# Optimization experiments

Measured on AMD Instinct MI355X. Metric: run time of the kernel, lower is better.

Reference implementation:

```python
import jax, jax.numpy as jnp
import numpy as np

IN_F, OUT_F, GROUP = 4096, 4096, 128
N_GROUPS = IN_F // GROUP  # 32


def setup_inputs() -> dict:
    key = jax.random.key(0)
    k1, k2, k3, k4, k5 = jax.random.split(key, 5)
    x = jax.random.normal(k1, (2, 1024, IN_F), dtype=jnp.float32)
    w_q = jax.random.randint(k2, (OUT_F, N_GROUPS, GROUP), -128, 128, dtype=jnp.int32)  # int8-range quantized weights
    s_w = jax.random.uniform(k3, (N_GROUPS, OUT_F), dtype=jnp.float32) * 0.01  # per-group, per-out-channel scales
    perm = jax.random.permutation(k4, IN_F).astype(jnp.int64)  # GPTQ activation-order permutation
    bias = jax.random.normal(k5, (OUT_F,), dtype=jnp.float32)
    return {"x": x, "w_q": w_q, "s_w": s_w, "perm": perm, "bias": bias}


def reference(x, w_q, s_w, perm, bias):
    prefix = x.shape[:-1]
    orig_dtype = x.dtype
    xf = x.reshape(-1, IN_F)          # (n, in)
    xf = xf[:, perm]                  # apply GPTQ permutation
    xf = xf.reshape(-1, N_GROUPS, GROUP).astype(jnp.float32)  # (n, g, k)
    wf = w_q.astype(jnp.float32)      # (o, g, k) dequant-to-fp32 weights (pre-scale)
    y_g = jnp.einsum('ngk,ogk->ngo', xf, wf)   # per-group partial products (n, g, o)
    y = jnp.sum(y_g * s_w[None, :, :], axis=1) # apply group scales, reduce groups -> (n, o)
    y = y + bias.astype(y.dtype)
    return y.reshape(*prefix, OUT_F).astype(orig_dtype)
```

## Files before the change

kernel.cpp:

```cpp
#include <hip/hip_runtime.h>
#include <hip/hip_bf16.h>
#include <stdint.h>

#define IN_F   4096
#define OUT_F  4096
#define M_ROWS 2048
#define NG     32
#define GRP    128

typedef int   v4i  __attribute__((ext_vector_type(4)));
typedef float f32x4 __attribute__((ext_vector_type(4)));

typedef const void __attribute__((address_space(1))) cv_g;
typedef void       __attribute__((address_space(3))) v_l;

__device__ __forceinline__ void async16(const void* g, void* l) {
  __builtin_amdgcn_global_load_lds((cv_g*)g, (v_l*)l, 16, 0, 0);
}

__device__ int g_perm_is64;

__global__ void decode_flag(const void* __restrict__ perm_raw) {
  if (threadIdx.x == 0 && blockIdx.x == 0) {
    const int* w = (const int*)perm_raw;
    int ok = 1;
    for (int j = 0; j < 32; ++j) {
      int lo = w[2 * j], hi = w[2 * j + 1];
      if (hi != 0 || lo < 0 || lo >= IN_F) { ok = 0; break; }
    }
    g_perm_is64 = ok;
  }
}

__global__ __launch_bounds__(256) void prep(const float* __restrict__ x,
                                            const int* __restrict__ w_q,
                                            const void* __restrict__ perm_raw,
                                            char* __restrict__ xq,
                                            char* __restrict__ w8,
                                            float* __restrict__ sxr) {
  __shared__ float sx[IN_F];
  __shared__ float red[4];
  __shared__ int sflag;
  const int b = blockIdx.x;
  const int t = threadIdx.x;

  if (b < M_ROWS) {
    const int m = b;
    const float* xr = x + (size_t)m * IN_F;
#pragma unroll
    for (int u = 0; u < 4; ++u) {
      int idx = (u * 256 + t) * 4;
      *(float4*)&sx[idx] = *(const float4*)&xr[idx];
    }
    if (t < 64) {
      const int* w = (const int*)perm_raw;
      int j = t & 31;
      int lo = w[2 * j], hi = w[2 * j + 1];
      int cond = (hi == 0 && lo >= 0 && lo < IN_F);
      unsigned long long bal = __ballot(cond);
      if (t == 0) sflag = (bal == ~0ull) ? 1 : 0;
    }
    __syncthreads();
    const int f = sflag;
    const long long* p64 = (const long long*)perm_raw;
    const int*       p32 = (const int*)perm_raw;
    const int jb = t * 16;
    float vals[16];
    float lmax = 0.f;
#pragma unroll
    for (int u = 0; u < 16; ++u) {
      int pj = f ? (int)p64[jb + u] : p32[jb + u];
      float v = sx[pj];
      vals[u] = v;
      lmax = fmaxf(lmax, fabsf(v));
    }
#pragma unroll
    for (int d = 1; d < 64; d <<= 1)
      lmax = fmaxf(lmax, __shfl_xor(lmax, d, 64));
    if ((t & 63) == 0) red[t >> 6] = lmax;
    __syncthreads();
    float rmax = fmaxf(fmaxf(red[0], red[1]), fmaxf(red[2], red[3]));
    float inv = (rmax > 0.f) ? 127.f / rmax : 0.f;
    if (t == 0) sxr[m] = rmax / 127.f;
    char q[16] __attribute__((aligned(16)));
#pragma unroll
    for (int u = 0; u < 16; ++u)
      q[u] = (char)__float2int_rn(vals[u] * inv);
    *(uint4*)(xq + (size_t)m * IN_F + jb) = *(const uint4*)q;
  } else {
    const int o  = b - M_ROWS;
    const int kb = t * 16;
    const int* wr = w_q + (size_t)o * IN_F + kb;
    int4 w0 = *(const int4*)(wr + 0);
    int4 w1 = *(const int4*)(wr + 4);
    int4 w2 = *(const int4*)(wr + 8);
    int4 w3 = *(const int4*)(wr + 12);
    char q[16] __attribute__((aligned(16)));
    q[0]=(char)w0.x; q[1]=(char)w0.y; q[2]=(char)w0.z; q[3]=(char)w0.w;
    q[4]=(char)w1.x; q[5]=(char)w1.y; q[6]=(char)w1.z; q[7]=(char)w1.w;
    q[8]=(char)w2.x; q[9]=(char)w2.y; q[10]=(char)w2.z; q[11]=(char)w2.w;
    q[12]=(char)w3.x; q[13]=(char)w3.y; q[14]=(char)w3.z; q[15]=(char)w3.w;
    *(uint4*)(w8 + (size_t)o * IN_F + kb) = *(const uint4*)q;
  }
}

__global__ __launch_bounds__(256, 2) void gemm_i8(
    const char* __restrict__ A,
    const char* __restrict__ B,
    const float* __restrict__ s_w,
    const float* __restrict__ sxr,
    const float* __restrict__ bias,
    float* __restrict__ C) {
  __shared__ char smem[2][32768];
  __shared__ unsigned short sws[NG * 128];

  const int tid  = threadIdx.x;
  const int wave = tid >> 6;
  const int lane = tid & 63;
  const int bm = blockIdx.y << 7;
  const int bn = blockIdx.x << 7;
  const int wm = (wave >> 1) << 6;
  const int wn = (wave & 1) << 6;
  const int lrow = lane & 15;
  const int quad = lane >> 4;

#pragma unroll
  for (int u = 0; u < 16; ++u) {
    int idx = u * 256 + tid;
    int g = idx >> 7, c = idx & 127;
    __hip_bfloat16 h = __float2bfloat16(s_w[(size_t)g * OUT_F + bn + c]);
    sws[idx] = *(unsigned short*)&h;
  }

  f32x4 accf[4][4] = {};

  const char* gp[8];
  int lofs[8];
#pragma unroll
  for (int h = 0; h < 8; ++h) {
    int c0 = (h * 4 + wave) * 64;
    int c  = c0 + lane;
    if (c < 1024) {
      int row = c >> 3;
      int kc  = (c & 7) ^ (row & 7);
      gp[h]   = A + (size_t)(bm + row) * IN_F + kc * 16;
      lofs[h] = c0 * 16;
    } else {
      int cb  = c - 1024;
      int row = cb >> 3;
      int kc  = (cb & 7) ^ (row & 7);
      gp[h]   = B + (size_t)(bn + row) * IN_F + kc * 16;
      lofs[h] = 16384 + (c0 - 1024) * 16;
    }
  }

  auto stage = [&](int p, int kn) {
#pragma unroll
    for (int h = 0; h < 8; ++h)
      async16(gp[h] + kn, &smem[p][lofs[h]]);
  };

  auto compute = [&](int p, int g) {
    const char* bufA = smem[p];
    const char* bufB = smem[p] + 16384;
    v4i acci[4][4] = {};
#pragma unroll
    for (int s = 0; s < 2; ++s) {
      v4i af[4], bf[4];
#pragma unroll
      for (int i = 0; i < 4; ++i) {
        int row = wm + i * 16 + lrow;
        af[i] = *(const v4i*)&bufA[row * 128 + (((s << 2) + quad) ^ (row & 7)) * 16];
      }
#pragma unroll
      for (int j = 0; j < 4; ++j) {
        int row = wn + j * 16 + lrow;
        bf[j] = *(const v4i*)&bufB[row * 128 + (((s << 2) + quad) ^ (row & 7)) * 16];
      }
#pragma unroll
      for (int i = 0; i < 4; ++i)
#pragma unroll
        for (int j = 0; j < 4; ++j)
          acci[i][j] = __builtin_amdgcn_mfma_i32_16x16x64_i8(af[i], bf[j], acci[i][j], 0, 0, 0);
    }
    float swv[4];
#pragma unroll
    for (int j = 0; j < 4; ++j) {
      unsigned int u = sws[g * 128 + wn + j * 16 + lrow];
      swv[j] = __uint_as_float(u << 16);
    }
#pragma unroll
    for (int i = 0; i < 4; ++i)
#pragma unroll
      for (int j = 0; j < 4; ++j)
#pragma unroll
        for (int r = 0; r < 4; ++r)
          accf[i][j][r] += swv[j] * (float)acci[i][j][r];
  };

  stage(0, 0);
  for (int k0 = 0; k0 < IN_F; k0 += 256) {
    __syncthreads();
    stage(1, k0 + 128);
    compute(0, k0 >> 7);
    __syncthreads();
    if (k0 + 256 < IN_F) stage(0, k0 + 256);
    compute(1, (k0 >> 7) + 1);
  }

#pragma unroll
  for (int i = 0; i < 4; ++i) {
    int r0 = bm + wm + i * 16 + quad * 4;
    float sxv[4];
#pragma unroll
    for (int r = 0; r < 4; ++r) sxv[r] = sxr[r0 + r];
#pragma unroll
    for (int j = 0; j < 4; ++j) {
      int col = bn + wn + j * 16 + lrow;
      float bv = bias[col];
#pragma unroll
      for (int r = 0; r < 4; ++r)
        C[(size_t)(r0 + r) * OUT_F + col] = sxv[r] * accf[i][j][r] + bv;
    }
  }
}

__global__ void naive_fallback(const float* __restrict__ x, const int* __restrict__ w_q,
                               const float* __restrict__ s_w, const void* __restrict__ perm_raw,
                               const float* __restrict__ bias, float* __restrict__ out) {
  int t = blockIdx.x * blockDim.x + threadIdx.x;
  int m = t >> 12;
  int o = t & 4095;
  const int f = g_perm_is64;
  const long long* p64 = (const long long*)perm_raw;
  const int*       p32 = (const int*)perm_raw;
  const float* xr = x + (size_t)m * IN_F;
  const int*   wr = w_q + (size_t)o * IN_F;
  float acc = 0.f;
  for (int g = 0; g < NG; ++g) {
    float part = 0.f;
    for (int k = 0; k < GRP; ++k) {
      int j = g * GRP + k;
      int pj = f ? (int)p64[j] : p32[j];
      part += xr[pj] * (float)wr[j];
    }
    acc += part * s_w[(size_t)g * OUT_F + o];
  }
  out[t] = acc + bias[o];
}

extern "C" void kernel_launch(void* const* d_in, const int* in_sizes, int n_in,
                              void* d_out, int out_size, void* d_ws, size_t ws_size,
                              hipStream_t stream) {
  const float* x    = (const float*)d_in[0];
  const int*   w_q  = (const int*)d_in[1];
  const float* s_w  = (const float*)d_in[2];
  const void*  perm = d_in[3];
  const float* bias = (const float*)d_in[4];
  float* out = (float*)d_out;

  const size_t xq_bytes = (size_t)M_ROWS * IN_F;
  const size_t w8_bytes = (size_t)OUT_F * IN_F;
  const size_t sx_bytes = (size_t)M_ROWS * sizeof(float);
  const size_t need = xq_bytes + w8_bytes + sx_bytes;

  if (ws_size < need) {
    decode_flag<<<1, 64, 0, stream>>>(perm);
    naive_fallback<<<(M_ROWS * OUT_F) / 256, 256, 0, stream>>>(x, w_q, s_w, perm, bias, out);
    return;
  }

  char*  xq  = (char*)d_ws;
  char*  w8  = (char*)d_ws + xq_bytes;
  float* sxr = (float*)((char*)d_ws + xq_bytes + w8_bytes);

  prep<<<M_ROWS + OUT_F, 256, 0, stream>>>(x, w_q, perm, xq, w8, sxr);

  dim3 grid(OUT_F / 128, M_ROWS / 128);
  gemm_i8<<<grid, 256, 0, stream>>>(xq, w8, s_w, sxr, bias, out);
}
```

Measured before the change: 193.0 us.

## Use 256x128 tiles with 512 threads and a triple-buffered async pipeline

```diff
diff --git a/kernel.cpp b/kernel.cpp
--- a/kernel.cpp
+++ b/kernel.cpp
@@ -7,6 +7,15 @@
 #define M_ROWS 2048
 #define NG     32
 #define GRP    128
+
+#define BM 256
+#define BN 128
+#define BK 128
+#define NTILES (IN_F / BK)
+#define ABYTES (BM * BK)
+#define BBYTES (BN * BK)
+#define BUFB   (ABYTES + BBYTES)
+#define ACHUNKS (ABYTES / 16)
 
 typedef int   v4i  __attribute__((ext_vector_type(4)));
 typedef float f32x4 __attribute__((ext_vector_type(4)));
@@ -104,20 +113,20 @@
   }
 }
 
-__global__ __launch_bounds__(256, 2) void gemm_i8(
+__global__ __launch_bounds__(512, 2) void gemm_i8(
     const char* __restrict__ A,
     const char* __restrict__ B,
     const float* __restrict__ s_w,
     const float* __restrict__ sxr,
     const float* __restrict__ bias,
     float* __restrict__ C) {
-  __shared__ char smem[2][32768];
-  __shared__ unsigned short sws[NG * 128];
+  __shared__ char smem[3][BUFB];
+  __shared__ unsigned short sws[NG * BN];
 
   const int tid  = threadIdx.x;
   const int wave = tid >> 6;
   const int lane = tid & 63;
-  const int bm = blockIdx.y << 7;
+  const int bm = blockIdx.y << 8;
   const int bn = blockIdx.x << 7;
   const int wm = (wave >> 1) << 6;
   const int wn = (wave & 1) << 6;
@@ -125,44 +134,51 @@
   const int quad = lane >> 4;
 
 #pragma unroll
-  for (int u = 0; u < 16; ++u) {
-    int idx = u * 256 + tid;
+  for (int u = 0; u < 8; ++u) {
+    int idx = u * 512 + tid;
     int g = idx >> 7, c = idx & 127;
     __hip_bfloat16 h = __float2bfloat16(s_w[(size_t)g * OUT_F + bn + c]);
     sws[idx] = *(unsigned short*)&h;
   }
 
-  f32x4 accf[4][4] = {};
-
-  const char* gp[8];
-  int lofs[8];
-#pragma unroll
-  for (int h = 0; h < 8; ++h) {
-    int c0 = (h * 4 + wave) * 64;
+  const char* gp[6];
+  int lofs[6];
+#pragma unroll
+  for (int h = 0; h < 6; ++h) {
+    int c0 = h * 512 + wave * 64;
     int c  = c0 + lane;
-    if (c < 1024) {
+    if (c0 < ACHUNKS) {
       int row = c >> 3;
       int kc  = (c & 7) ^ (row & 7);
       gp[h]   = A + (size_t)(bm + row) * IN_F + kc * 16;
       lofs[h] = c0 * 16;
     } else {
-      int cb  = c - 1024;
+      int cb  = c - ACHUNKS;
       int row = cb >> 3;
       int kc  = (cb & 7) ^ (row & 7);
       gp[h]   = B + (size_t)(bn + row) * IN_F + kc * 16;
-      lofs[h] = 16384 + (c0 - 1024) * 16;
-    }
-  }
-
-  auto stage = [&](int p, int kn) {
-#pragma unroll
-    for (int h = 0; h < 8; ++h)
-      async16(gp[h] + kn, &smem[p][lofs[h]]);
-  };
-
-  auto compute = [&](int p, int g) {
-    const char* bufA = smem[p];
-    const char* bufB = smem[p] + 16384;
+      lofs[h] = ABYTES + (c0 - ACHUNKS) * 16;
+    }
+  }
+
+  f32x4 accf[4][4] = {};
+
+#pragma unroll
+  for (int h = 0; h < 6; ++h) async16(gp[h], &smem[0][lofs[h]]);
+#pragma unroll
+  for (int h = 0; h < 6; ++h) async16(gp[h] + BK, &smem[1][lofs[h]]);
+  asm volatile("s_waitcnt vmcnt(6) lgkmcnt(0)" ::: "memory");
+  __builtin_amdgcn_s_barrier();
+  asm volatile("" ::: "memory");
+
+  int bufsel = 0;
+  for (int g = 0; g < NTILES; ++g) {
+    const char* bufA = smem[bufsel];
+    const char* bufB = bufA + ABYTES;
+    const int  stg   = (bufsel + 2 >= 3) ? bufsel - 1 : bufsel + 2;
+    const bool do_stage = (g + 2 < NTILES);
+    const int  kofs  = (g + 2) * BK;
+
     v4i acci[4][4] = {};
 #pragma unroll
     for (int s = 0; s < 2; ++s) {
@@ -170,23 +186,37 @@
 #pragma unroll
       for (int i = 0; i < 4; ++i) {
         int row = wm + i * 16 + lrow;
-        af[i] = *(const v4i*)&bufA[row * 128 + (((s << 2) + quad) ^ (row & 7)) * 16];
+        af[i] = *(const v4i*)&bufA[row * BK + ((((s << 2) + quad) ^ (row & 7)) << 4)];
       }
 #pragma unroll
       for (int j = 0; j < 4; ++j) {
         int row = wn + j * 16 + lrow;
-        bf[j] = *(const v4i*)&bufB[row * 128 + (((s << 2) + quad) ^ (row & 7)) * 16];
+        bf[j] = *(const v4i*)&bufB[row * BK + ((((s << 2) + quad) ^ (row & 7)) << 4)];
       }
+      if (do_stage) {
+#pragma unroll
+        for (int h = s * 3; h < s * 3 + 3; ++h)
+          async16(gp[h] + kofs, &smem[stg][lofs[h]]);
+      }
+      __builtin_amdgcn_s_barrier();
+      asm volatile("" ::: "memory");
+      __builtin_amdgcn_s_setprio(1);
 #pragma unroll
       for (int i = 0; i < 4; ++i)
 #pragma unroll
         for (int j = 0; j < 4; ++j)
           acci[i][j] = __builtin_amdgcn_mfma_i32_16x16x64_i8(af[i], bf[j], acci[i][j], 0, 0, 0);
-    }
+      __builtin_amdgcn_s_setprio(0);
+      if (s == 0) {
+        __builtin_amdgcn_s_barrier();
+        asm volatile("" ::: "memory");
+      }
+    }
+
     float swv[4];
 #pragma unroll
     for (int j = 0; j < 4; ++j) {
-      unsigned int u = sws[g * 128 + wn + j * 16 + lrow];
+      unsigned int u = sws[g * BN + wn + j * 16 + lrow];
       swv[j] = __uint_as_float(u << 16);
     }
 #pragma unroll
@@ -196,16 +226,14 @@
 #pragma unroll
         for (int r = 0; r < 4; ++r)
           accf[i][j][r] += swv[j] * (float)acci[i][j][r];
-  };
-
-  stage(0, 0);
-  for (int k0 = 0; k0 < IN_F; k0 += 256) {
-    __syncthreads();
-    stage(1, k0 + 128);
-    compute(0, k0 >> 7);
-    __syncthreads();
-    if (k0 + 256 < IN_F) stage(0, k0 + 256);
-    compute(1, (k0 >> 7) + 1);
+
+    if (g < NTILES - 1) {
+      if (g < NTILES - 2) asm volatile("s_waitcnt vmcnt(6)" ::: "memory");
+      else                asm volatile("s_waitcnt vmcnt(0)" ::: "memory");
+      __builtin_amdgcn_s_barrier();
+      asm volatile("" ::: "memory");
+    }
+    bufsel = (bufsel + 1 == 3) ? 0 : bufsel + 1;
   }
 
 #pragma unroll
@@ -276,6 +304,6 @@
 
   prep<<<M_ROWS + OUT_F, 256, 0, stream>>>(x, w_q, perm, xq, w8, sxr);
 
-  dim3 grid(OUT_F / 128, M_ROWS / 128);
-  gemm_i8<<<grid, 256, 0, stream>>>(xq, w8, s_w, sxr, bias, out);
-}
+  dim3 grid(OUT_F / BN, M_ROWS / BM);
+  gemm_i8<<<grid, 512, 0, stream>>>(xq, w8, s_w, sxr, bias, out);
+}
```

New measurement: 191.4 us. Within noise of the previous version (-0.8%).

## Restructure int8 GEMM main loop into a software-pipelined, single-barrier schedule

Applied to the files above, without the earlier changes.

```diff
diff --git a/kernel.cpp b/kernel.cpp
--- a/kernel.cpp
+++ b/kernel.cpp
@@ -111,8 +111,9 @@
     const float* __restrict__ sxr,
     const float* __restrict__ bias,
     float* __restrict__ C) {
-  __shared__ char smem[2][32768];
-  __shared__ unsigned short sws[NG * 128];
+  __shared__ __attribute__((aligned(16))) char lds[73728];
+  unsigned short* sws = (unsigned short*)lds;
+  const int BUF0 = 8192, BUF1 = 40960;
 
   const int tid  = threadIdx.x;
   const int wave = tid >> 6;
@@ -132,15 +133,13 @@
     sws[idx] = *(unsigned short*)&h;
   }
 
-  f32x4 accf[4][4] = {};
-
   const char* gp[8];
   int lofs[8];
 #pragma unroll
   for (int h = 0; h < 8; ++h) {
     int c0 = (h * 4 + wave) * 64;
     int c  = c0 + lane;
-    if (c < 1024) {
+    if (c0 < 1024) {
       int row = c >> 3;
       int kc  = (c & 7) ^ (row & 7);
       gp[h]   = A + (size_t)(bm + row) * IN_F + kc * 16;
@@ -154,35 +153,21 @@
     }
   }
 
-  auto stage = [&](int p, int kn) {
-#pragma unroll
-    for (int h = 0; h < 8; ++h)
-      async16(gp[h] + kn, &smem[p][lofs[h]]);
-  };
-
-  auto compute = [&](int p, int g) {
-    const char* bufA = smem[p];
-    const char* bufB = smem[p] + 16384;
-    v4i acci[4][4] = {};
-#pragma unroll
-    for (int s = 0; s < 2; ++s) {
-      v4i af[4], bf[4];
-#pragma unroll
-      for (int i = 0; i < 4; ++i) {
-        int row = wm + i * 16 + lrow;
-        af[i] = *(const v4i*)&bufA[row * 128 + (((s << 2) + quad) ^ (row & 7)) * 16];
-      }
-#pragma unroll
-      for (int j = 0; j < 4; ++j) {
-        int row = wn + j * 16 + lrow;
-        bf[j] = *(const v4i*)&bufB[row * 128 + (((s << 2) + quad) ^ (row & 7)) * 16];
-      }
-#pragma unroll
-      for (int i = 0; i < 4; ++i)
-#pragma unroll
-        for (int j = 0; j < 4; ++j)
-          acci[i][j] = __builtin_amdgcn_mfma_i32_16x16x64_i8(af[i], bf[j], acci[i][j], 0, 0, 0);
-    }
+  const int xlo = lrow & 7;
+  int aoff[2][4], boff[2][4];
+#pragma unroll
+  for (int s = 0; s < 2; ++s) {
+    int slot = (((s << 2) | quad) ^ xlo) << 4;
+#pragma unroll
+    for (int i = 0; i < 4; ++i) aoff[s][i] = (wm + i * 16 + lrow) * 128 + slot;
+#pragma unroll
+    for (int j = 0; j < 4; ++j) boff[s][j] = 16384 + (wn + j * 16 + lrow) * 128 + slot;
+  }
+
+  f32x4 accf[4][4] = {};
+  v4i   acci[4][4] = {};
+
+  auto rescale = [&](int g) {
     float swv[4];
 #pragma unroll
     for (int j = 0; j < 4; ++j) {
@@ -192,21 +177,58 @@
 #pragma unroll
     for (int i = 0; i < 4; ++i)
 #pragma unroll
-      for (int j = 0; j < 4; ++j)
+      for (int j = 0; j < 4; ++j) {
 #pragma unroll
         for (int r = 0; r < 4; ++r)
           accf[i][j][r] += swv[j] * (float)acci[i][j][r];
+        acci[i][j] = (v4i){0, 0, 0, 0};
+      }
   };
 
-  stage(0, 0);
-  for (int k0 = 0; k0 < IN_F; k0 += 256) {
-    __syncthreads();
-    stage(1, k0 + 128);
-    compute(0, k0 >> 7);
-    __syncthreads();
-    if (k0 + 256 < IN_F) stage(0, k0 + 256);
-    compute(1, (k0 >> 7) + 1);
-  }
+  auto tile = [&](int t, int pbase, int qbase, bool doPrev, bool doStage) {
+    v4i af0[4], bf0[4], af1[4], bf1[4];
+#pragma unroll
+    for (int i = 0; i < 4; ++i) af0[i] = *(const v4i*)&lds[pbase + aoff[0][i]];
+#pragma unroll
+    for (int j = 0; j < 4; ++j) bf0[j] = *(const v4i*)&lds[pbase + boff[0][j]];
+#pragma unroll
+    for (int i = 0; i < 4; ++i) af1[i] = *(const v4i*)&lds[pbase + aoff[1][i]];
+#pragma unroll
+    for (int j = 0; j < 4; ++j) bf1[j] = *(const v4i*)&lds[pbase + boff[1][j]];
+    if (doStage) {
+      const int kn = (t + 1) * GRP;
+#pragma unroll
+      for (int h = 0; h < 8; ++h) async16(gp[h] + kn, &lds[qbase + lofs[h]]);
+    }
+    if (doPrev) rescale(t - 1);
+    __builtin_amdgcn_s_setprio(1);
+#pragma unroll
+    for (int i = 0; i < 4; ++i)
+#pragma unroll
+      for (int j = 0; j < 4; ++j)
+        acci[i][j] = __builtin_amdgcn_mfma_i32_16x16x64_i8(af0[i], bf0[j], acci[i][j], 0, 0, 0);
+#pragma unroll
+    for (int i = 0; i < 4; ++i)
+#pragma unroll
+      for (int j = 0; j < 4; ++j)
+        acci[i][j] = __builtin_amdgcn_mfma_i32_16x16x64_i8(af1[i], bf1[j], acci[i][j], 0, 0, 0);
+    __builtin_amdgcn_s_setprio(0);
+    if (doStage) asm volatile("s_waitcnt vmcnt(0)" ::: "memory");
+    __builtin_amdgcn_s_barrier();
+    asm volatile("" ::: "memory");
+  };
+
+#pragma unroll
+  for (int h = 0; h < 8; ++h) async16(gp[h], &lds[BUF0 + lofs[h]]);
+  asm volatile("s_waitcnt vmcnt(0) lgkmcnt(0)" ::: "memory");
+  __builtin_amdgcn_s_barrier();
+  asm volatile("" ::: "memory");
+
+  for (int it = 0; it < 16; ++it) {
+    tile(2 * it,     BUF0, BUF1, it > 0, true);
+    tile(2 * it + 1, BUF1, BUF0, true,   it < 15);
+  }
+  rescale(NG - 1);
 
 #pragma unroll
   for (int i = 0; i < 4; ++i) {
```

New measurement: 212.5 us. 1.1x slower.

## Load B fragments directly to registers and software-pipeline the int8 GEMM main loop

Applied to the files above, without the earlier changes.

```diff
diff --git a/kernel.cpp b/kernel.cpp
--- a/kernel.cpp
+++ b/kernel.cpp
@@ -111,8 +111,9 @@
     const float* __restrict__ sxr,
     const float* __restrict__ bias,
     float* __restrict__ C) {
-  __shared__ char smem[2][32768];
-  __shared__ unsigned short sws[NG * 128];
+  __shared__ __attribute__((aligned(16))) char lds[40960];
+  unsigned short* sws = (unsigned short*)lds;
+  const int BUF0 = 8192, BUF1 = 24576;
 
   const int tid  = threadIdx.x;
   const int wave = tid >> 6;
@@ -132,57 +133,23 @@
     sws[idx] = *(unsigned short*)&h;
   }
 
-  f32x4 accf[4][4] = {};
-
-  const char* gp[8];
-  int lofs[8];
-#pragma unroll
-  for (int h = 0; h < 8; ++h) {
+  const char* gp[4];
+  int lofs[4];
+#pragma unroll
+  for (int h = 0; h < 4; ++h) {
     int c0 = (h * 4 + wave) * 64;
     int c  = c0 + lane;
-    if (c < 1024) {
-      int row = c >> 3;
-      int kc  = (c & 7) ^ (row & 7);
-      gp[h]   = A + (size_t)(bm + row) * IN_F + kc * 16;
-      lofs[h] = c0 * 16;
-    } else {
-      int cb  = c - 1024;
-      int row = cb >> 3;
-      int kc  = (cb & 7) ^ (row & 7);
-      gp[h]   = B + (size_t)(bn + row) * IN_F + kc * 16;
-      lofs[h] = 16384 + (c0 - 1024) * 16;
-    }
-  }
-
-  auto stage = [&](int p, int kn) {
-#pragma unroll
-    for (int h = 0; h < 8; ++h)
-      async16(gp[h] + kn, &smem[p][lofs[h]]);
-  };
-
-  auto compute = [&](int p, int g) {
-    const char* bufA = smem[p];
-    const char* bufB = smem[p] + 16384;
-    v4i acci[4][4] = {};
-#pragma unroll
-    for (int s = 0; s < 2; ++s) {
-      v4i af[4], bf[4];
-#pragma unroll
-      for (int i = 0; i < 4; ++i) {
-        int row = wm + i * 16 + lrow;
-        af[i] = *(const v4i*)&bufA[row * 128 + (((s << 2) + quad) ^ (row & 7)) * 16];
-      }
-#pragma unroll
-      for (int j = 0; j < 4; ++j) {
-        int row = wn + j * 16 + lrow;
-        bf[j] = *(const v4i*)&bufB[row * 128 + (((s << 2) + quad) ^ (row & 7)) * 16];
-      }
-#pragma unroll
-      for (int i = 0; i < 4; ++i)
-#pragma unroll
-        for (int j = 0; j < 4; ++j)
-          acci[i][j] = __builtin_amdgcn_mfma_i32_16x16x64_i8(af[i], bf[j], acci[i][j], 0, 0, 0);
-    }
+    int row = c >> 3;
+    int kc  = (c & 7) ^ (row & 7);
+    gp[h]   = A + (size_t)(bm + row) * IN_F + kc * 16;
+    lofs[h] = c0 * 16;
+  }
+
+  f32x4 accf[4][4] = {};
+  v4i   acci[4][4] = {};
+  v4i   bfX[2][4], bfY[2][4];
+
+  auto rescale = [&](int g) {
     float swv[4];
 #pragma unroll
     for (int j = 0; j < 4; ++j) {
@@ -192,21 +159,76 @@
 #pragma unroll
     for (int i = 0; i < 4; ++i)
 #pragma unroll
-      for (int j = 0; j < 4; ++j)
+      for (int j = 0; j < 4; ++j) {
 #pragma unroll
         for (int r = 0; r < 4; ++r)
           accf[i][j][r] += swv[j] * (float)acci[i][j][r];
+        acci[i][j] = (v4i){0, 0, 0, 0};
+      }
   };
 
-  stage(0, 0);
-  for (int k0 = 0; k0 < IN_F; k0 += 256) {
-    __syncthreads();
-    stage(1, k0 + 128);
-    compute(0, k0 >> 7);
-    __syncthreads();
-    if (k0 + 256 < IN_F) stage(0, k0 + 256);
-    compute(1, (k0 >> 7) + 1);
-  }
+  const char* Brow = B + (size_t)(bn + wn + lrow) * IN_F + (quad << 4);
+
+#define TILE(T, PB, QB, BC, BN_, DOPREV, DOSTAGE)                              \
+  {                                                                            \
+    if (DOSTAGE) {                                                             \
+      const int kn = (T + 1) * GRP;                                            \
+      _Pragma("unroll")                                                        \
+      for (int h = 0; h < 4; ++h) async16(gp[h] + kn, &lds[QB + lofs[h]]);     \
+      __builtin_amdgcn_sched_barrier(0);                                       \
+      _Pragma("unroll")                                                        \
+      for (int s = 0; s < 2; ++s)                                              \
+        _Pragma("unroll")                                                      \
+        for (int j = 0; j < 4; ++j)                                            \
+          BN_[s][j] = *(const v4i*)(Brow + (size_t)(j * 16) * IN_F +           \
+                                    (T + 1) * GRP + (s << 6));                 \
+      __builtin_amdgcn_sched_barrier(0);                                       \
+    }                                                                          \
+    if (DOPREV) rescale((T) - 1);                                              \
+    _Pragma("unroll")                                                          \
+    for (int s = 0; s < 2; ++s) {                                              \
+      v4i af[4];                                                               \
+      _Pragma("unroll")                                                        \
+      for (int i = 0; i < 4; ++i) {                                            \
+        int row = wm + i * 16 + lrow;                                          \
+        af[i] = *(const v4i*)&lds[PB + row * 128 +                             \
+                                  ((((s << 2) | quad) ^ (lrow & 7)) << 4)];    \
+      }                                                                        \
+      __builtin_amdgcn_s_setprio(1);                                           \
+      _Pragma("unroll")                                                        \
+      for (int i = 0; i < 4; ++i)                                              \
+        _Pragma("unroll")                                                      \
+        for (int j = 0; j < 4; ++j)                                            \
+          acci[i][j] = __builtin_amdgcn_mfma_i32_16x16x64_i8(                  \
+              af[i], BC[s][j], acci[i][j], 0, 0, 0);                           \
+      __builtin_amdgcn_s_setprio(0);                                           \
+    }                                                                          \
+    if (DOSTAGE) {                                                             \
+      asm volatile("s_waitcnt vmcnt(8)" ::: "memory");                         \
+      __builtin_amdgcn_s_barrier();                                            \
+      asm volatile("" ::: "memory");                                           \
+    }                                                                          \
+  }
+
+#pragma unroll
+  for (int h = 0; h < 4; ++h) async16(gp[h], &lds[BUF0 + lofs[h]]);
+  __builtin_amdgcn_sched_barrier(0);
+#pragma unroll
+  for (int s = 0; s < 2; ++s)
+#pragma unroll
+    for (int j = 0; j < 4; ++j)
+      bfX[s][j] = *(const v4i*)(Brow + (size_t)(j * 16) * IN_F + (s << 6));
+  __builtin_amdgcn_sched_barrier(0);
+  asm volatile("s_waitcnt vmcnt(8) lgkmcnt(0)" ::: "memory");
+  __builtin_amdgcn_s_barrier();
+  asm volatile("" ::: "memory");
+
+  for (int it = 0; it < 16; ++it) {
+    TILE(2 * it,     BUF0, BUF1, bfX, bfY, (it > 0), true);
+    TILE(2 * it + 1, BUF1, BUF0, bfY, bfX, true,     (it < 15));
+  }
+  rescale(NG - 1);
+#undef TILE
 
 #pragma unroll
   for (int i = 0; i < 4; ++i) {
```

New measurement: 243.4 us. 1.26x slower.
